# Kernel tuning notes

Hardware: AMD Instinct MI355X
Metric: run time of the kernel (lower is better)

The kernel has to match this reference:

```python
import jax, jax.numpy as jnp
import numpy as np

N = 768
D = 2
MARGIN = 0.01


def setup_inputs() -> dict:
    key = jax.random.key(0)
    k1, _ = jax.random.split(key)
    node_pos = jax.random.normal(k1, (N, D), dtype=jnp.float32)
    batch = jnp.zeros((N,), dtype=jnp.int32)  # unused by the loss math
    return {"node_pos": node_pos, "batch": batch}


def reference(node_pos, batch):
    n = node_pos.shape[0]
    # all unordered node pairs (equivalent to torch.combinations(arange(n), r=2))
    i_idx, j_idx = jnp.triu_indices(n, k=1)
    pi = node_pos[i_idx]              # [m, d]
    pj = node_pos[j_idx]              # [m, d]
    midpoints = 0.5 * (pi + pj)       # [m, d]
    radii = 0.5 * jnp.linalg.norm(pi - pj, axis=1) + MARGIN  # [m]
    # Euclidean cdist(node_pos [n,d], midpoints [m,d]) via expanded quadratic form
    x_sq = jnp.sum(node_pos * node_pos, axis=1)          # [n]
    m_sq = jnp.sum(midpoints * midpoints, axis=1)        # [m]
    cross = node_pos @ midpoints.T                       # [n, m]
    dist_sq = x_sq[:, None] + m_sq[None, :] - 2.0 * cross
    distances = jnp.sqrt(jnp.maximum(dist_sq, 0.0))      # [n, m]
    energy = jnp.square(jax.nn.relu(radii[None, :] - distances))
    return jnp.mean(energy)
```

## Files before the change

### kernel.cpp

```cpp
#include <hip/hip_runtime.h>

#define NN 768
#define NPAIRS ((NN * (NN - 1)) / 2)
#define MARGIN_F 0.01f
#define CHUNK 256
#define NCHUNK 3

__global__ __launch_bounds__(256) void gg_pre(const float* __restrict__ pos,
                                              float4* __restrict__ nd) {
    int i = blockIdx.x * blockDim.x + threadIdx.x;
    if (i < NN) {
        float x = pos[2 * i], y = pos[2 * i + 1];
        nd[i] = make_float4(x, y, fmaf(x, x, y * y), 0.0f);
    }
}

__global__ __launch_bounds__(256) void gg_main(const float* __restrict__ pos,
                                               const float4* __restrict__ nd,
                                               float* __restrict__ out,
                                               float inv_total) {
    int p = blockIdx.x * blockDim.x + threadIdx.x;
    int kbase = blockIdx.y * CHUNK;
    float acc = 0.0f;

    if (p < NPAIRS) {
        const float A = 2.0f * NN - 1.0f;
        float disc = A * A - 8.0f * (float)p;
        int i = (int)((A - __builtin_amdgcn_sqrtf(disc)) * 0.5f);
        if (i < 0) i = 0;
        if (i > NN - 2) i = NN - 2;
        while (((i + 1) * (2 * NN - 1 - (i + 1))) / 2 <= p) ++i;
        while ((i * (2 * NN - 1 - i)) / 2 > p) --i;
        int off = (i * (2 * NN - 1 - i)) / 2;
        int j = i + 1 + (p - off);

        float xix = pos[2 * i], xiy = pos[2 * i + 1];
        float xjx = pos[2 * j], xjy = pos[2 * j + 1];
        float mx = 0.5f * (xix + xjx);
        float my = 0.5f * (xiy + xjy);
        float ddx = xix - xjx, ddy = xiy - xjy;
        float r  = 0.5f * __builtin_amdgcn_sqrtf(fmaf(ddx, ddx, ddy * ddy)) + MARGIN_F;
        float cx = -2.0f * mx;
        float cy = -2.0f * my;
        float cc = fmaf(mx, mx, my * my);

        #pragma unroll 8
        for (int k = kbase; k < kbase + CHUNK; ++k) {
            float4 n = nd[k];
            float c  = cc + n.z;
            float d2 = fmaf(n.x, cx, fmaf(n.y, cy, c));
            float d  = __builtin_amdgcn_sqrtf(d2);
            float t  = fmaxf(r - d, 0.0f);
            acc = fmaf(t, t, acc);
        }
    }

    for (int o = 32; o > 0; o >>= 1) acc += __shfl_down(acc, o);

    __shared__ float ws[4];
    int lane = threadIdx.x & 63;
    int wid  = threadIdx.x >> 6;
    if (lane == 0) ws[wid] = acc;
    __syncthreads();
    if (threadIdx.x == 0) {
        float s = (ws[0] + ws[1]) + (ws[2] + ws[3]);
        atomicAdd(out, s * inv_total);
    }
}

extern "C" void kernel_launch(void* const* d_in, const int* in_sizes, int n_in,
                              void* d_out, int out_size, void* d_ws, size_t ws_size,
                              hipStream_t stream) {
    const float* pos = (const float*)d_in[0];
    float* out = (float*)d_out;
    float4* nd = (float4*)d_ws;

    hipMemsetAsync(out, 0, sizeof(float), stream);
    gg_pre<<<NCHUNK, 256, 0, stream>>>(pos, nd);

    double total = (double)NN * (double)NPAIRS;
    float inv_total = (float)(1.0 / total);

    dim3 grid((NPAIRS + 255) / 256, NCHUNK);
    gg_main<<<grid, 256, 0, stream>>>(pos, nd, out, inv_total);
}
```

Before: 111.1 us.

## Use packed float2 math over SoA node arrays and split node range finer

```diff
diff --git a/kernel.cpp b/kernel.cpp
--- a/kernel.cpp
+++ b/kernel.cpp
@@ -1,27 +1,31 @@
 #include <hip/hip_runtime.h>
+
+typedef float v2f __attribute__((ext_vector_type(2)));
 
 #define NN 768
 #define NPAIRS ((NN * (NN - 1)) / 2)
 #define MARGIN_F 0.01f
-#define CHUNK 256
-#define NCHUNK 3
+#define CHUNK 128
+#define NCHUNK 6
 
 __global__ __launch_bounds__(256) void gg_pre(const float* __restrict__ pos,
-                                              float4* __restrict__ nd) {
+                                              float* __restrict__ ws) {
     int i = blockIdx.x * blockDim.x + threadIdx.x;
     if (i < NN) {
         float x = pos[2 * i], y = pos[2 * i + 1];
-        nd[i] = make_float4(x, y, fmaf(x, x, y * y), 0.0f);
+        ws[i]            = x;
+        ws[NN + i]       = y;
+        ws[2 * NN + i]   = fmaf(x, x, y * y);
     }
 }
 
 __global__ __launch_bounds__(256) void gg_main(const float* __restrict__ pos,
-                                               const float4* __restrict__ nd,
+                                               const float* __restrict__ ws,
                                                float* __restrict__ out,
                                                float inv_total) {
     int p = blockIdx.x * blockDim.x + threadIdx.x;
     int kbase = blockIdx.y * CHUNK;
-    float acc = 0.0f;
+    v2f acc2 = {0.0f, 0.0f};
 
     if (p < NPAIRS) {
         const float A = 2.0f * NN - 1.0f;
@@ -40,30 +44,46 @@
         float my = 0.5f * (xiy + xjy);
         float ddx = xix - xjx, ddy = xiy - xjy;
         float r  = 0.5f * __builtin_amdgcn_sqrtf(fmaf(ddx, ddx, ddy * ddy)) + MARGIN_F;
-        float cx = -2.0f * mx;
-        float cy = -2.0f * my;
-        float cc = fmaf(mx, mx, my * my);
+
+        v2f cx2 = {-2.0f * mx, -2.0f * mx};
+        v2f cy2 = {-2.0f * my, -2.0f * my};
+        v2f cc2;  cc2.x = fmaf(mx, mx, my * my);  cc2.y = cc2.x;
+        v2f rv  = {r, r};
+        v2f neg1 = {-1.0f, -1.0f};
+        v2f zero = {0.0f, 0.0f};
+
+        const v2f* xs2 = (const v2f*)(ws + kbase);
+        const v2f* ys2 = (const v2f*)(ws + NN + kbase);
+        const v2f* zs2 = (const v2f*)(ws + 2 * NN + kbase);
 
         #pragma unroll 8
-        for (int k = kbase; k < kbase + CHUNK; ++k) {
-            float4 n = nd[k];
-            float c  = cc + n.z;
-            float d2 = fmaf(n.x, cx, fmaf(n.y, cy, c));
-            float d  = __builtin_amdgcn_sqrtf(d2);
-            float t  = fmaxf(r - d, 0.0f);
-            acc = fmaf(t, t, acc);
+        for (int t = 0; t < CHUNK / 2; ++t) {
+            v2f xv = xs2[t];
+            v2f yv = ys2[t];
+            v2f zv = zs2[t];
+            v2f c  = zv + cc2;
+            c      = __builtin_elementwise_fma(yv, cy2, c);
+            v2f d2 = __builtin_elementwise_fma(xv, cx2, c);
+            v2f d;
+            d.x = __builtin_amdgcn_sqrtf(d2.x);
+            d.y = __builtin_amdgcn_sqrtf(d2.y);
+            v2f tt = __builtin_elementwise_fma(d, neg1, rv);
+            tt = __builtin_elementwise_max(tt, zero);
+            acc2 = __builtin_elementwise_fma(tt, tt, acc2);
         }
     }
 
+    float acc = acc2.x + acc2.y;
+
     for (int o = 32; o > 0; o >>= 1) acc += __shfl_down(acc, o);
 
-    __shared__ float ws[4];
+    __shared__ float wsum[4];
     int lane = threadIdx.x & 63;
     int wid  = threadIdx.x >> 6;
-    if (lane == 0) ws[wid] = acc;
+    if (lane == 0) wsum[wid] = acc;
     __syncthreads();
     if (threadIdx.x == 0) {
-        float s = (ws[0] + ws[1]) + (ws[2] + ws[3]);
+        float s = (wsum[0] + wsum[1]) + (wsum[2] + wsum[3]);
         atomicAdd(out, s * inv_total);
     }
 }
@@ -73,14 +93,14 @@
                               hipStream_t stream) {
     const float* pos = (const float*)d_in[0];
     float* out = (float*)d_out;
-    float4* nd = (float4*)d_ws;
+    float* ws  = (float*)d_ws;
 
     hipMemsetAsync(out, 0, sizeof(float), stream);
-    gg_pre<<<NCHUNK, 256, 0, stream>>>(pos, nd);
+    gg_pre<<<NCHUNK, 256, 0, stream>>>(pos, ws);
 
     double total = (double)NN * (double)NPAIRS;
     float inv_total = (float)(1.0 / total);
 
     dim3 grid((NPAIRS + 255) / 256, NCHUNK);
-    gg_main<<<grid, 256, 0, stream>>>(pos, nd, out, inv_total);
+    gg_main<<<grid, 256, 0, stream>>>(pos, ws, out, inv_total);
 }
```

After: 149.8 us. 1.35x slower.
